# Kernel optimization log

Hardware: AMD Instinct MI355X
Metric: run time of the kernel (lower is better)

The kernel has to match this reference:

```python
import jax, jax.numpy as jnp
import numpy as np

N = 50000
E = 800000
D_IN, D_HID, D_OUT = 128, 128, 64


def setup_inputs() -> dict:
    key = jax.random.key(0)
    ks = jax.random.split(key, 8)
    x = jax.random.normal(ks[0], (N, D_IN), dtype=jnp.float32)
    edge_index = jax.random.randint(ks[1], (2, E), 0, N, dtype=jnp.int64)
    # SAGEConv params: lin_l (neighbors, with bias), lin_r (root, no bias)
    s1 = 1.0 / np.sqrt(D_IN)
    s2 = 1.0 / np.sqrt(D_HID)
    W1_l = jax.random.uniform(ks[2], (D_IN, D_HID), jnp.float32, -s1, s1)
    b1 = jnp.zeros((D_HID,), jnp.float32)
    W1_r = jax.random.uniform(ks[3], (D_IN, D_HID), jnp.float32, -s1, s1)
    W2_l = jax.random.uniform(ks[4], (D_HID, D_OUT), jnp.float32, -s2, s2)
    b2 = jnp.zeros((D_OUT,), jnp.float32)
    W2_r = jax.random.uniform(ks[5], (D_HID, D_OUT), jnp.float32, -s2, s2)
    return {"x": x, "edge_index": edge_index, "W1_l": W1_l, "b1": b1,
            "W1_r": W1_r, "W2_l": W2_l, "b2": b2, "W2_r": W2_r}


def _sage_conv(x, src, dst, Wl, b, Wr, num_nodes):
    # mean aggregation over incoming edges (src -> dst)
    msgs = x[src]                                              # [E, d]
    agg = jax.ops.segment_sum(msgs, dst, num_segments=num_nodes)
    cnt = jax.ops.segment_sum(jnp.ones((src.shape[0],), x.dtype), dst,
                              num_segments=num_nodes)
    mean = agg / jnp.clip(cnt, 1.0)[:, None]                   # [N, d]
    return mean @ Wl + b + x @ Wr


def reference(x, edge_index, W1_l, b1, W1_r, W2_l, b2, W2_r):
    src, dst = edge_index[0], edge_index[1]
    n = x.shape[0]
    h = jax.nn.relu(_sage_conv(x, src, dst, W1_l, b1, W1_r, n))
    # dropout p=0.5 is identity in eval mode (training=False)
    return _sage_conv(h, src, dst, W2_l, b2, W2_r, n)
```

## Files before the change

kernel.cpp:

```cpp
#include <hip/hip_runtime.h>
#include <hip/hip_bf16.h>

typedef __hip_bfloat16 bf16;
typedef __attribute__((ext_vector_type(8))) short short8;
typedef __attribute__((ext_vector_type(4))) float floatx4;
typedef __attribute__((ext_vector_type(2))) float floatx2;
typedef unsigned short u16;
typedef unsigned char u8;

#define NNODES 50000
#define NEDGES 800000
#define D_IN  128
#define D_HID 128
#define D_OUT 64
#define SLOTS 64
#define NRANGE 8
#define RSPAN (NNODES / NRANGE)
#define EXB 512

__device__ __forceinline__ float bfbits2f(unsigned int u) {
    return __uint_as_float(u << 16);
}
__device__ __forceinline__ float b2f(bf16 v) { return __bfloat162float(v); }
__device__ __forceinline__ unsigned short f2bfbits(float f) {
    bf16 b = __float2bfloat16(f);
    return *(unsigned short*)&b;
}
__device__ __forceinline__ u8 f2fp8(float f) {
    return (u8)(__builtin_amdgcn_cvt_pk_fp8_f32(f, 0.f, 0, false) & 0xFF);
}
__device__ __forceinline__ float ld(const void* p, long long idx, int isf32) {
    if (isf32) return ((const float*)p)[idx];
    return b2f(((const bf16*)p)[idx]);
}

__global__ void k_setup(int* __restrict__ cnt, int n,
                        const unsigned int* __restrict__ ei_words,
                        const unsigned int* __restrict__ w_words,
                        int* __restrict__ flags,
                        const void* __restrict__ x,
                        const void* __restrict__ W1l, const void* __restrict__ W1r,
                        const void* __restrict__ W2l, const void* __restrict__ W2r,
                        bf16* __restrict__ p1l, bf16* __restrict__ p1r,
                        bf16* __restrict__ p2l, bf16* __restrict__ p2r,
                        unsigned int* __restrict__ x8,
                        u16* __restrict__ src16, u16* __restrict__ dst16) {
    int b = blockIdx.x;
    if (b < 128) {
        if (b == 0) {
            __shared__ int cnt_zero, cnt_bf;
            if (threadIdx.x == 0) { cnt_zero = 0; cnt_bf = 0; }
            __syncthreads();
            int t = threadIdx.x;
            unsigned int we = ei_words[2 * t + 1];
            if (we == 0u) atomicAdd(&cnt_zero, 1);
            unsigned int ww = w_words[t];
            unsigned int lowexp = (ww >> 7) & 0xFFu;
            if (lowexp >= 0x60u && lowexp <= 0x7Bu) atomicAdd(&cnt_bf, 1);
            __syncthreads();
            if (threadIdx.x == 0) {
                flags[0] = (cnt_zero >= 240) ? 1 : 0;
                flags[1] = (cnt_bf >= 192) ? 0 : 1;
            }
        }
        int i = b * blockDim.x + threadIdx.x;
        int stride = 128 * blockDim.x;
        for (; i < n; i += stride) cnt[i] = 0;
        return;
    }
    if (b < 664) {
        if (b >= 152) {
            __shared__ int cz;
            if (threadIdx.x == 0) cz = 0;
            __syncthreads();
            {
                unsigned int we = ei_words[2 * threadIdx.x + 1];
                if (we == 0u) atomicAdd(&cz, 1);
            }
            __syncthreads();
            int is64 = (cz >= 240);
            const int* ei = (const int*)ei_words;
            for (int e = (b - 152) * 256 + threadIdx.x; e < NEDGES; e += EXB * 256) {
                int s, d;
                if (is64) { s = ei[2 * e]; d = ei[2 * (NEDGES + e)]; }
                else      { s = ei[e];     d = ei[NEDGES + e]; }
                src16[e] = (u16)s;
                dst16[e] = (u16)d;
            }
            return;
        }
        __shared__ int cnt_bf2;
        if (threadIdx.x == 0) cnt_bf2 = 0;
        __syncthreads();
        {
            unsigned int ww = w_words[threadIdx.x];
            unsigned int lowexp = (ww >> 7) & 0xFFu;
            if (lowexp >= 0x60u && lowexp <= 0x7Bu) atomicAdd(&cnt_bf2, 1);
        }
        __syncthreads();
        int isf32 = (cnt_bf2 >= 192) ? 0 : 1;
        int t = (b - 128) * 256 + threadIdx.x;
        if (t >= 6144) return;
        const void* Wm; bf16* dst; int NT; int base;
        if (t < 2048)      { Wm = W1l; dst = p1l; NT = 8; base = t; }
        else if (t < 4096) { Wm = W1r; dst = p1r; NT = 8; base = t - 2048; }
        else if (t < 5120) { Wm = W2l; dst = p2l; NT = 4; base = t - 4096; }
        else               { Wm = W2r; dst = p2r; NT = 4; base = t - 5120; }
        int lane = base & 63;
        int kt = (base >> 6) & 3;
        int nt = base >> 8;
        int Nmat = NT * 16;
        int krow = kt * 32 + ((lane >> 4) * 8);
        int col = nt * 16 + (lane & 15);
        #pragma unroll
        for (int j = 0; j < 8; j++) {
            float v = ld(Wm, (long long)(krow + j) * Nmat + col, isf32);
            dst[(((nt * 4 + kt) * 64 + lane) * 8) + j] = __float2bfloat16(v);
        }
        return;
    }
    __shared__ int cnt_bf2;
    if (threadIdx.x == 0) cnt_bf2 = 0;
    __syncthreads();
    {
        unsigned int ww = w_words[threadIdx.x];
        unsigned int lowexp = (ww >> 7) & 0xFFu;
        if (lowexp >= 0x60u && lowexp <= 0x7Bu) atomicAdd(&cnt_bf2, 1);
    }
    __syncthreads();
    int isf32 = (cnt_bf2 >= 192) ? 0 : 1;
    const long long NU32 = (long long)NNODES * D_IN / 4;
    long long i = (long long)(b - 664) * 256 + threadIdx.x;
    long long stride = (long long)(gridDim.x - 664) * 256;
    if (isf32) {
        const float4* xf = (const float4*)x;
        for (; i < NU32; i += stride) {
            float4 f = xf[i];
            unsigned int w0 = __builtin_amdgcn_cvt_pk_fp8_f32(f.x, f.y, 0, false);
            w0 = __builtin_amdgcn_cvt_pk_fp8_f32(f.z, f.w, w0, true);
            x8[i] = w0;
        }
    } else {
        const ushort4* xb = (const ushort4*)x;
        for (; i < NU32; i += stride) {
            ushort4 s = xb[i];
            float f0 = bfbits2f(s.x), f1 = bfbits2f(s.y);
            float f2 = bfbits2f(s.z), f3 = bfbits2f(s.w);
            unsigned int w0 = __builtin_amdgcn_cvt_pk_fp8_f32(f0, f1, 0, false);
            w0 = __builtin_amdgcn_cvt_pk_fp8_f32(f2, f3, w0, true);
            x8[i] = w0;
        }
    }
}

__global__ void k_edges(const u16* __restrict__ dst16, const u16* __restrict__ src16,
                        u16* __restrict__ csr16, int* __restrict__ cnt) {
    int b = blockIdx.x;
    int lo = (b & (NRANGE - 1)) * RSPAN;
    int hi = lo + RSPAN;
    int gi = b >> 3;
    int stride = (gridDim.x >> 3) * 256;
    for (int e = gi * 256 + threadIdx.x; e < NEDGES; e += stride) {
        int d = (int)dst16[e];
        if (d >= lo && d < hi) {
            int s = (int)src16[e];
            int rank = atomicAdd(&cnt[d], 1);
            if (rank < SLOTS) csr16[((size_t)d << 6) + rank] = (u16)s;
        }
    }
}

__device__ __forceinline__ void g16m(const unsigned int* __restrict__ x8w, int my,
                                     int j, int cnt2, int h, int c,
                                     float& a0, float& a1, float& a2, float& a3) {
    int jb = j + h * 8;
    int i0 = __shfl(my, jb + 0), i1 = __shfl(my, jb + 1);
    int i2 = __shfl(my, jb + 2), i3 = __shfl(my, jb + 3);
    int i4 = __shfl(my, jb + 4), i5 = __shfl(my, jb + 5);
    int i6 = __shfl(my, jb + 6), i7 = __shfl(my, jb + 7);
    unsigned int u0 = x8w[((unsigned)i0 << 5) + c];
    unsigned int u1 = x8w[((unsigned)i1 << 5) + c];
    unsigned int u2 = x8w[((unsigned)i2 << 5) + c];
    unsigned int u3 = x8w[((unsigned)i3 << 5) + c];
    unsigned int u4 = x8w[((unsigned)i4 << 5) + c];
    unsigned int u5 = x8w[((unsigned)i5 << 5) + c];
    unsigned int u6 = x8w[((unsigned)i6 << 5) + c];
    unsigned int u7 = x8w[((unsigned)i7 << 5) + c];
    float m0 = (jb + 0 < cnt2) ? 1.f : 0.f;
    float m1 = (jb + 1 < cnt2) ? 1.f : 0.f;
    float m2 = (jb + 2 < cnt2) ? 1.f : 0.f;
    float m3 = (jb + 3 < cnt2) ? 1.f : 0.f;
    float m4 = (jb + 4 < cnt2) ? 1.f : 0.f;
    float m5 = (jb + 5 < cnt2) ? 1.f : 0.f;
    float m6 = (jb + 6 < cnt2) ? 1.f : 0.f;
    float m7 = (jb + 7 < cnt2) ? 1.f : 0.f;
    floatx2 l0 = __builtin_amdgcn_cvt_pk_f32_fp8(u0, false);
    floatx2 h0 = __builtin_amdgcn_cvt_pk_f32_fp8(u0, true);
    floatx2 l1 = __builtin_amdgcn_cvt_pk_f32_fp8(u1, false);
    floatx2 h1 = __builtin_amdgcn_cvt_pk_f32_fp8(u1, true);
    floatx2 l2 = __builtin_amdgcn_cvt_pk_f32_fp8(u2, false);
    floatx2 h2 = __builtin_amdgcn_cvt_pk_f32_fp8(u2, true);
    floatx2 l3 = __builtin_amdgcn_cvt_pk_f32_fp8(u3, false);
    floatx2 h3 = __builtin_amdgcn_cvt_pk_f32_fp8(u3, true);
    floatx2 l4 = __builtin_amdgcn_cvt_pk_f32_fp8(u4, false);
    floatx2 h4 = __builtin_amdgcn_cvt_pk_f32_fp8(u4, true);
    floatx2 l5 = __builtin_amdgcn_cvt_pk_f32_fp8(u5, false);
    floatx2 h5 = __builtin_amdgcn_cvt_pk_f32_fp8(u5, true);
    floatx2 l6 = __builtin_amdgcn_cvt_pk_f32_fp8(u6, false);
    floatx2 h6 = __builtin_amdgcn_cvt_pk_f32_fp8(u6, true);
    floatx2 l7 = __builtin_amdgcn_cvt_pk_f32_fp8(u7, false);
    floatx2 h7 = __builtin_amdgcn_cvt_pk_f32_fp8(u7, true);
    a0 += m0 * l0.x; a1 += m0 * l0.y; a2 += m0 * h0.x; a3 += m0 * h0.y;
    a0 += m1 * l1.x; a1 += m1 * l1.y; a2 += m1 * h1.x; a3 += m1 * h1.y;
    a0 += m2 * l2.x; a1 += m2 * l2.y; a2 += m2 * h2.x; a3 += m2 * h2.y;
    a0 += m3 * l3.x; a1 += m3 * l3.y; a2 += m3 * h3.x; a3 += m3 * h3.y;
    a0 += m4 * l4.x; a1 += m4 * l4.y; a2 += m4 * h4.x; a3 += m4 * h4.y;
    a0 += m5 * l5.x; a1 += m5 * l5.y; a2 += m5 * h5.x; a3 += m5 * h5.y;
    a0 += m6 * l6.x; a1 += m6 * l6.y; a2 += m6 * h6.x; a3 += m6 * h6.y;
    a0 += m7 * l7.x; a1 += m7 * l7.y; a2 += m7 * h7.x; a3 += m7 * h7.y;
}

__global__ __launch_bounds__(512) void k_l1fused(
        const u16* __restrict__ csr16, const int* __restrict__ cnt,
        const void* __restrict__ x, const unsigned int* __restrict__ x8w,
        const int* __restrict__ flags,
        const bf16* __restrict__ p1l, const bf16* __restrict__ p1r,
        const bf16* __restrict__ p2l, const bf16* __restrict__ p2r,
        const void* __restrict__ b1, const void* __restrict__ b2v,
        u8* __restrict__ h28, float* __restrict__ hrf) {
    __shared__ bf16 ms[16][136];
    __shared__ bf16 xs[16][136];
    __shared__ bf16 hs[16][136];
    __shared__ u8 h2s8[16][72];
    __shared__ float hrs[16][68];
    int t = threadIdx.x;
    int w = t >> 6;
    int l = t & 63;
    int nb = blockIdx.x * 16;
    int isf32 = flags[1];
    int r0 = w * 2, r1 = r0 + 1;
    int h = l >> 5;
    int c = l & 31;

    int mya = (int)csr16[((size_t)(nb + r0) << 6) + l];
    int myb = (int)csr16[((size_t)(nb + r1) << 6) + l];
    int cw = cnt[nb + r0 + min(l, 1)];

    {
        long long ro0 = (long long)(nb + r0) * D_IN + 2 * l;
        long long ro1 = (long long)(nb + r1) * D_IN + 2 * l;
        unsigned int px0, px1;
        if (isf32) {
            float2 v0 = *(const float2*)((const float*)x + ro0);
            float2 v1 = *(const float2*)((const float*)x + ro1);
            px0 = ((unsigned int)f2bfbits(v0.y) << 16) | f2bfbits(v0.x);
            px1 = ((unsigned int)f2bfbits(v1.y) << 16) | f2bfbits(v1.x);
        } else {
            px0 = *(const unsigned int*)((const bf16*)x + ro0);
            px1 = *(const unsigned int*)((const bf16*)x + ro1);
        }
        *(unsigned int*)((bf16*)&xs[r0][0] + 2 * l) = px0;
        *(unsigned int*)((bf16*)&xs[r1][0] + 2 * l) = px1;
    }

    int da = __shfl(cw, 0), db = __shfl(cw, 1);
    int ca = min(SLOTS, da), cb = min(SLOTS, db);

    float aa0 = 0.f, aa1 = 0.f, aa2 = 0.f, aa3 = 0.f;
    float bb0 = 0.f, bb1 = 0.f, bb2 = 0.f, bb3 = 0.f;
    {
        int mx = max(ca, cb);
        for (int j = 0; j < mx; j += 16) {
            g16m(x8w, mya, j, ca, h, c, aa0, aa1, aa2, aa3);
            g16m(x8w, myb, j, cb, h, c, bb0, bb1, bb2, bb3);
        }
    }
    aa0 += __shfl_xor(aa0, 32); aa1 += __shfl_xor(aa1, 32);
    aa2 += __shfl_xor(aa2, 32); aa3 += __shfl_xor(aa3, 32);
    bb0 += __shfl_xor(bb0, 32); bb1 += __shfl_xor(bb1, 32);
    bb2 += __shfl_xor(bb2, 32); bb3 += __shfl_xor(bb3, 32);
    if (l < 32) {
        float inv = 1.0f / fmaxf((float)da, 1.0f);
        uint2 pk;
        pk.x = ((unsigned int)f2bfbits(aa1 * inv) << 16) | f2bfbits(aa0 * inv);
        pk.y = ((unsigned int)f2bfbits(aa3 * inv) << 16) | f2bfbits(aa2 * inv);
        *(uint2*)((bf16*)&ms[r0][0] + (c << 2)) = pk;
    } else {
        float inv = 1.0f / fmaxf((float)db, 1.0f);
        uint2 pk;
        pk.x = ((unsigned int)f2bfbits(bb1 * inv) << 16) | f2bfbits(bb0 * inv);
        pk.y = ((unsigned int)f2bfbits(bb3 * inv) << 16) | f2bfbits(bb2 * inv);
        *(uint2*)((bf16*)&ms[r1][0] + (c << 2)) = pk;
    }
    __syncthreads();

    int m = l & 15;
    int quad = l >> 4;
    floatx4 acc0 = {0.f, 0.f, 0.f, 0.f};
    #pragma unroll
    for (int kt = 0; kt < 4; kt++) {
        short8 amv = *(const short8*)&ms[m][kt * 32 + quad * 8];
        short8 axv = *(const short8*)&xs[m][kt * 32 + quad * 8];
        short8 bl0 = *(const short8*)(p1l + (((w * 4 + kt) * 64 + l) * 8));
        short8 br0 = *(const short8*)(p1r + (((w * 4 + kt) * 64 + l) * 8));
        acc0 = __builtin_amdgcn_mfma_f32_16x16x32_bf16(amv, bl0, acc0, 0, 0, 0);
        acc0 = __builtin_amdgcn_mfma_f32_16x16x32_bf16(axv, br0, acc0, 0, 0, 0);
    }
    int c0 = w * 16 + m;
    float bias0 = ld(b1, c0, isf32);
    #pragma unroll
    for (int r = 0; r < 4; r++) {
        hs[quad * 4 + r][c0] = __float2bfloat16(fmaxf(acc0[r] + bias0, 0.f));
    }
    __syncthreads();
    if (w < 4) {
        floatx4 acc2 = {0.f, 0.f, 0.f, 0.f};
        floatx4 acc3 = {0.f, 0.f, 0.f, 0.f};
        #pragma unroll
        for (int kt = 0; kt < 4; kt++) {
            short8 ah = *(const short8*)&hs[m][kt * 32 + quad * 8];
            short8 bw = *(const short8*)(p2l + (((w * 4 + kt) * 64 + l) * 8));
            short8 bz = *(const short8*)(p2r + (((w * 4 + kt) * 64 + l) * 8));
            acc2 = __builtin_amdgcn_mfma_f32_16x16x32_bf16(ah, bw, acc2, 0, 0, 0);
            acc3 = __builtin_amdgcn_mfma_f32_16x16x32_bf16(ah, bz, acc3, 0, 0, 0);
        }
        int c2 = w * 16 + m;
        float bias2 = ld(b2v, c2, isf32);
        #pragma unroll
        for (int r = 0; r < 4; r++) {
            h2s8[quad * 4 + r][c2] = f2fp8(acc2[r]);
            hrs[quad * 4 + r][c2] = acc3[r] + bias2;
        }
    }
    __syncthreads();
    if (t < 128) {
        int node = t >> 3, col0 = (t & 7) * 8;
        uint2 v = *(const uint2*)&h2s8[node][col0];
        *(uint2*)(h28 + (long long)(nb + node) * D_OUT + col0) = v;
    }
    if (t < 256) {
        int node = t >> 4, col0 = (t & 15) * 4;
        float4 v = *(const float4*)&hrs[node][col0];
        *(float4*)(hrf + (long long)(nb + node) * D_OUT + col0) = v;
    }
}

__device__ __forceinline__ void a16m(const unsigned int* __restrict__ h32, int my,
                                     int j, int cnt2, int g, int c,
                                     float& a0, float& a1, float& a2, float& a3) {
    int jj0 = j + g, jj1 = j + 4 + g, jj2 = j + 8 + g, jj3 = j + 12 + g;
    int i0 = __shfl(my, jj0);
    int i1 = __shfl(my, jj1);
    int i2 = __shfl(my, jj2);
    int i3 = __shfl(my, jj3);
    unsigned int u0 = h32[(size_t)i0 * 16 + c];
    unsigned int u1 = h32[(size_t)i1 * 16 + c];
    unsigned int u2 = h32[(size_t)i2 * 16 + c];
    unsigned int u3 = h32[(size_t)i3 * 16 + c];
    float m0 = (jj0 < cnt2) ? 1.f : 0.f;
    float m1 = (jj1 < cnt2) ? 1.f : 0.f;
    float m2 = (jj2 < cnt2) ? 1.f : 0.f;
    float m3 = (jj3 < cnt2) ? 1.f : 0.f;
    floatx2 l0 = __builtin_amdgcn_cvt_pk_f32_fp8(u0, false);
    floatx2 h0 = __builtin_amdgcn_cvt_pk_f32_fp8(u0, true);
    floatx2 l1 = __builtin_amdgcn_cvt_pk_f32_fp8(u1, false);
    floatx2 h1 = __builtin_amdgcn_cvt_pk_f32_fp8(u1, true);
    floatx2 l2 = __builtin_amdgcn_cvt_pk_f32_fp8(u2, false);
    floatx2 h2 = __builtin_amdgcn_cvt_pk_f32_fp8(u2, true);
    floatx2 l3 = __builtin_amdgcn_cvt_pk_f32_fp8(u3, false);
    floatx2 h3 = __builtin_amdgcn_cvt_pk_f32_fp8(u3, true);
    a0 += m0 * l0.x; a1 += m0 * l0.y; a2 += m0 * h0.x; a3 += m0 * h0.y;
    a0 += m1 * l1.x; a1 += m1 * l1.y; a2 += m1 * h1.x; a3 += m1 * h1.y;
    a0 += m2 * l2.x; a1 += m2 * l2.y; a2 += m2 * h2.x; a3 += m2 * h2.y;
    a0 += m3 * l3.x; a1 += m3 * l3.y; a2 += m3 * h3.x; a3 += m3 * h3.y;
}

__global__ void k_agg2g(const u16* __restrict__ csr16, const int* __restrict__ cnt,
                        const u8* __restrict__ h28, const float* __restrict__ hrf,
                        const int* __restrict__ flags, void* __restrict__ out) {
    int t = threadIdx.x;
    int lane = t & 63;
    int n0 = blockIdx.x * 8 + (t >> 6) * 2;
    int n1 = n0 + 1;
    int g = lane >> 4;
    int c = lane & 15;
    const unsigned int* h32 = (const unsigned int*)h28;

    int mya = (int)csr16[((size_t)n0 << 6) + lane];
    int myb = (int)csr16[((size_t)n1 << 6) + lane];
    int cw = cnt[n0 + min(lane, 1)];
    float4 hr = {0.f, 0.f, 0.f, 0.f};
    if (lane < 32) {
        int nn = (lane < 16) ? n0 : n1;
        hr = *(const float4*)&hrf[(size_t)nn * D_OUT + (c << 2)];
    }
    int da = __shfl(cw, 0), db = __shfl(cw, 1);
    int ca = min(SLOTS, da), cb = min(SLOTS, db);

    float a0 = 0.f, a1 = 0.f, a2 = 0.f, a3 = 0.f;
    float b0 = 0.f, b1 = 0.f, b2 = 0.f, b3 = 0.f;
    {
        int mx = max(ca, cb);
        for (int j = 0; j < mx; j += 16) {
            a16m(h32, mya, j, ca, g, c, a0, a1, a2, a3);
            a16m(h32, myb, j, cb, g, c, b0, b1, b2, b3);
        }
    }
    a0 += __shfl_xor(a0, 32); a0 += __shfl_xor(a0, 16);
    a1 += __shfl_xor(a1, 32); a1 += __shfl_xor(a1, 16);
    a2 += __shfl_xor(a2, 32); a2 += __shfl_xor(a2, 16);
    a3 += __shfl_xor(a3, 32); a3 += __shfl_xor(a3, 16);
    b0 += __shfl_xor(b0, 32); b0 += __shfl_xor(b0, 16);
    b1 += __shfl_xor(b1, 32); b1 += __shfl_xor(b1, 16);
    b2 += __shfl_xor(b2, 32); b2 += __shfl_xor(b2, 16);
    b3 += __shfl_xor(b3, 32); b3 += __shfl_xor(b3, 16);
    if (lane < 16) {
        float inv = 1.0f / fmaxf((float)da, 1.0f);
        float o0 = a0 * inv + hr.x;
        float o1 = a1 * inv + hr.y;
        float o2 = a2 * inv + hr.z;
        float o3 = a3 * inv + hr.w;
        if (flags[1]) {
            float4 v = {o0, o1, o2, o3};
            *(float4*)((float*)out + (size_t)n0 * D_OUT + (c << 2)) = v;
        } else {
            uint2 v;
            v.x = ((unsigned int)f2bfbits(o1) << 16) | f2bfbits(o0);
            v.y = ((unsigned int)f2bfbits(o3) << 16) | f2bfbits(o2);
            *(uint2*)((bf16*)out + (size_t)n0 * D_OUT + (c << 2)) = v;
        }
    } else if (lane < 32) {
        float inv = 1.0f / fmaxf((float)db, 1.0f);
        float o0 = b0 * inv + hr.x;
        float o1 = b1 * inv + hr.y;
        float o2 = b2 * inv + hr.z;
        float o3 = b3 * inv + hr.w;
        if (flags[1]) {
            float4 v = {o0, o1, o2, o3};
            *(float4*)((float*)out + (size_t)n1 * D_OUT + (c << 2)) = v;
        } else {
            uint2 v;
            v.x = ((unsigned int)f2bfbits(o1) << 16) | f2bfbits(o0);
            v.y = ((unsigned int)f2bfbits(o3) << 16) | f2bfbits(o2);
            *(uint2*)((bf16*)out + (size_t)n1 * D_OUT + (c << 2)) = v;
        }
    }
}

extern "C" void kernel_launch(void* const* d_in, const int* in_sizes, int n_in,
                              void* d_out, int out_size, void* d_ws, size_t ws_size,
                              hipStream_t stream) {
    const void* x   = d_in[0];
    const int*  ei  = (const int*)d_in[1];
    const void* W1l = d_in[2];
    const void* b1  = d_in[3];
    const void* W1r = d_in[4];
    const void* W2l = d_in[5];
    const void* b2v = d_in[6];
    const void* W2r = d_in[7];

    const int N = NNODES;
    const int E = NEDGES;

    int*          flags     = (int*)d_ws;
    int*          cnt       = flags + 4;
    u16*          csr16     = (u16*)(cnt + N);
    u16*          src16     = csr16 + (size_t)N * SLOTS;
    u16*          dst16     = src16 + E;
    bf16*         p1l       = (bf16*)(dst16 + E);
    bf16*         p1r       = p1l + 16384;
    bf16*         p2l       = p1r + 16384;
    bf16*         p2r       = p2l + 8192;
    unsigned int* x8        = (unsigned int*)(p2r + 8192);
    u8*           h28       = (u8*)(x8 + (size_t)N * D_IN / 4);
    float*        hrf       = (float*)(h28 + (size_t)N * D_OUT);

    k_setup<<<664 + 1024, 256, 0, stream>>>(cnt, N, (const unsigned int*)ei,
                                            (const unsigned int*)W1l, flags, x,
                                            W1l, W1r, W2l, W2r,
                                            p1l, p1r, p2l, p2r, x8, src16, dst16);
    k_edges<<<2048, 256, 0, stream>>>(dst16, src16, csr16, cnt);
    k_l1fused<<<N / 16, 512, 0, stream>>>(csr16, cnt, x, x8, flags,
                                          p1l, p1r, p2l, p2r, b1, b2v, h28, hrf);
    k_agg2g<<<N / 8, 256, 0, stream>>>(csr16, cnt, h28, hrf, flags, d_out);
}
```

Baseline: 182.1 us.

## Pack edge src/dst into one word and shrink layer-1 blocks to eight nodes

Edge indices are now packed as one 32-bit word (src in the high half, dst in the low half), so the bucketing kernel does one load per edge instead of two separate 16-bit array reads. The fused layer-1 kernel moves from 16 nodes with 512 threads per block to 8 nodes with 256 threads, and each wave now computes two 16-column output tiles. This doubles the block count to raise occupancy and shrinks shared memory per block. The cost is that the 16-row MFMA tiles are only half used (rows 8-15 are wasted), and the compute-to-load ratio for the weight fragments gets worse.

```diff
diff --git a/kernel.cpp b/kernel.cpp
--- a/kernel.cpp
+++ b/kernel.cpp
@@ -44,7 +44,7 @@
                         bf16* __restrict__ p1l, bf16* __restrict__ p1r,
                         bf16* __restrict__ p2l, bf16* __restrict__ p2r,
                         unsigned int* __restrict__ x8,
-                        u16* __restrict__ src16, u16* __restrict__ dst16) {
+                        unsigned int* __restrict__ sd32) {
     int b = blockIdx.x;
     if (b < 128) {
         if (b == 0) {
@@ -84,8 +84,7 @@
                 int s, d;
                 if (is64) { s = ei[2 * e]; d = ei[2 * (NEDGES + e)]; }
                 else      { s = ei[e];     d = ei[NEDGES + e]; }
-                src16[e] = (u16)s;
-                dst16[e] = (u16)d;
+                sd32[e] = ((unsigned int)s << 16) | (unsigned int)d;
             }
             return;
         }
@@ -153,7 +152,7 @@
     }
 }
 
-__global__ void k_edges(const u16* __restrict__ dst16, const u16* __restrict__ src16,
+__global__ void k_edges(const unsigned int* __restrict__ sd32,
                         u16* __restrict__ csr16, int* __restrict__ cnt) {
     int b = blockIdx.x;
     int lo = (b & (NRANGE - 1)) * RSPAN;
@@ -161,11 +160,11 @@
     int gi = b >> 3;
     int stride = (gridDim.x >> 3) * 256;
     for (int e = gi * 256 + threadIdx.x; e < NEDGES; e += stride) {
-        int d = (int)dst16[e];
+        unsigned int sd = sd32[e];
+        int d = (int)(sd & 0xFFFFu);
         if (d >= lo && d < hi) {
-            int s = (int)src16[e];
             int rank = atomicAdd(&cnt[d], 1);
-            if (rank < SLOTS) csr16[((size_t)d << 6) + rank] = (u16)s;
+            if (rank < SLOTS) csr16[((size_t)d << 6) + rank] = (u16)(sd >> 16);
         }
     }
 }
@@ -220,7 +219,7 @@
     a0 += m7 * l7.x; a1 += m7 * l7.y; a2 += m7 * h7.x; a3 += m7 * h7.y;
 }
 
-__global__ __launch_bounds__(512) void k_l1fused(
+__global__ __launch_bounds__(256) void k_l1fused(
         const u16* __restrict__ csr16, const int* __restrict__ cnt,
         const void* __restrict__ x, const unsigned int* __restrict__ x8w,
         const int* __restrict__ flags,
@@ -231,12 +230,12 @@
     __shared__ bf16 ms[16][136];
     __shared__ bf16 xs[16][136];
     __shared__ bf16 hs[16][136];
-    __shared__ u8 h2s8[16][72];
-    __shared__ float hrs[16][68];
+    __shared__ u8 h2s8[8][72];
+    __shared__ float hrs[8][68];
     int t = threadIdx.x;
     int w = t >> 6;
     int l = t & 63;
-    int nb = blockIdx.x * 16;
+    int nb = blockIdx.x * 8;
     int isf32 = flags[1];
     int r0 = w * 2, r1 = r0 + 1;
     int h = l >> 5;
@@ -296,24 +295,34 @@
 
     int m = l & 15;
     int quad = l >> 4;
+    int nt0 = w * 2, nt1 = nt0 + 1;
     floatx4 acc0 = {0.f, 0.f, 0.f, 0.f};
+    floatx4 acc1 = {0.f, 0.f, 0.f, 0.f};
     #pragma unroll
     for (int kt = 0; kt < 4; kt++) {
         short8 amv = *(const short8*)&ms[m][kt * 32 + quad * 8];
         short8 axv = *(const short8*)&xs[m][kt * 32 + quad * 8];
-        short8 bl0 = *(const short8*)(p1l + (((w * 4 + kt) * 64 + l) * 8));
-        short8 br0 = *(const short8*)(p1r + (((w * 4 + kt) * 64 + l) * 8));
+        short8 bl0 = *(const short8*)(p1l + (((nt0 * 4 + kt) * 64 + l) * 8));
+        short8 br0 = *(const short8*)(p1r + (((nt0 * 4 + kt) * 64 + l) * 8));
         acc0 = __builtin_amdgcn_mfma_f32_16x16x32_bf16(amv, bl0, acc0, 0, 0, 0);
         acc0 = __builtin_amdgcn_mfma_f32_16x16x32_bf16(axv, br0, acc0, 0, 0, 0);
-    }
-    int c0 = w * 16 + m;
+        short8 bl1 = *(const short8*)(p1l + (((nt1 * 4 + kt) * 64 + l) * 8));
+        short8 br1 = *(const short8*)(p1r + (((nt1 * 4 + kt) * 64 + l) * 8));
+        acc1 = __builtin_amdgcn_mfma_f32_16x16x32_bf16(amv, bl1, acc1, 0, 0, 0);
+        acc1 = __builtin_amdgcn_mfma_f32_16x16x32_bf16(axv, br1, acc1, 0, 0, 0);
+    }
+    int c0 = nt0 * 16 + m;
+    int c1 = nt1 * 16 + m;
     float bias0 = ld(b1, c0, isf32);
+    float bias1 = ld(b1, c1, isf32);
     #pragma unroll
     for (int r = 0; r < 4; r++) {
-        hs[quad * 4 + r][c0] = __float2bfloat16(fmaxf(acc0[r] + bias0, 0.f));
+        int row = quad * 4 + r;
+        hs[row][c0] = __float2bfloat16(fmaxf(acc0[r] + bias0, 0.f));
+        hs[row][c1] = __float2bfloat16(fmaxf(acc1[r] + bias1, 0.f));
     }
     __syncthreads();
-    if (w < 4) {
+    {
         floatx4 acc2 = {0.f, 0.f, 0.f, 0.f};
         floatx4 acc3 = {0.f, 0.f, 0.f, 0.f};
         #pragma unroll
@@ -328,17 +337,20 @@
         float bias2 = ld(b2v, c2, isf32);
         #pragma unroll
         for (int r = 0; r < 4; r++) {
-            h2s8[quad * 4 + r][c2] = f2fp8(acc2[r]);
-            hrs[quad * 4 + r][c2] = acc3[r] + bias2;
+            int row = quad * 4 + r;
+            if (row < 8) {
+                h2s8[row][c2] = f2fp8(acc2[r]);
+                hrs[row][c2] = acc3[r] + bias2;
+            }
         }
     }
     __syncthreads();
-    if (t < 128) {
+    if (t < 64) {
         int node = t >> 3, col0 = (t & 7) * 8;
         uint2 v = *(const uint2*)&h2s8[node][col0];
         *(uint2*)(h28 + (long long)(nb + node) * D_OUT + col0) = v;
     }
-    if (t < 256) {
+    if (t < 128) {
         int node = t >> 4, col0 = (t & 15) * 4;
         float4 v = *(const float4*)&hrs[node][col0];
         *(float4*)(hrf + (long long)(nb + node) * D_OUT + col0) = v;
@@ -465,9 +477,8 @@
     int*          flags     = (int*)d_ws;
     int*          cnt       = flags + 4;
     u16*          csr16     = (u16*)(cnt + N);
-    u16*          src16     = csr16 + (size_t)N * SLOTS;
-    u16*          dst16     = src16 + E;
-    bf16*         p1l       = (bf16*)(dst16 + E);
+    unsigned int* sd32      = (unsigned int*)(csr16 + (size_t)N * SLOTS);
+    bf16*         p1l       = (bf16*)(sd32 + E);
     bf16*         p1r       = p1l + 16384;
     bf16*         p2l       = p1r + 16384;
     bf16*         p2r       = p2l + 8192;
@@ -478,9 +489,9 @@
     k_setup<<<664 + 1024, 256, 0, stream>>>(cnt, N, (const unsigned int*)ei,
                                             (const unsigned int*)W1l, flags, x,
                                             W1l, W1r, W2l, W2r,
-                                            p1l, p1r, p2l, p2r, x8, src16, dst16);
-    k_edges<<<2048, 256, 0, stream>>>(dst16, src16, csr16, cnt);
-    k_l1fused<<<N / 16, 512, 0, stream>>>(csr16, cnt, x, x8, flags,
-                                          p1l, p1r, p2l, p2r, b1, b2v, h28, hrf);
+                                            p1l, p1r, p2l, p2r, x8, sd32);
+    k_edges<<<2048, 256, 0, stream>>>(sd32, csr16, cnt);
+    k_l1fused<<<N / 8, 256, 0, stream>>>(csr16, cnt, x, x8, flags,
+                                         p1l, p1r, p2l, p2r, b1, b2v, h28, hrf);
     k_agg2g<<<N / 8, 256, 0, stream>>>(csr16, cnt, h28, hrf, flags, d_out);
 }
```

Result: no change. 185.4 us (+1.8%).
